# Optimization experiments

Measured on AMD Instinct MI355X. Metric: run time of the kernel, lower is better.

## Reference

```python
import jax, jax.numpy as jnp
import numpy as np

B, N, M, Wlen = 4, 20000, 64, 8


def setup_inputs() -> dict:
    key = jax.random.key(0)
    k1, k2, k3, k4 = jax.random.split(key, 4)
    a0 = jax.random.uniform(k1, (B, N), dtype=jnp.float32)
    W = 0.01 * jax.random.normal(k2, (M, M), dtype=jnp.float32)
    X1 = jax.random.randint(k3, (M, N, Wlen, 2), 0, N, dtype=jnp.int64)
    X2 = jax.random.randint(k4, (M, N, Wlen, 2), 0, N, dtype=jnp.int64)
    return {"a0": a0, "W": W, "X1": X1, "X2": X2, "T": 2}


def f_clause_stack(a, X):
    # a: [B,n], X: [m,n,w,2] -> [B,m,n]
    y1 = a[:, X[..., 0]]  # [B,m,n,w] gather
    y2 = a[:, X[..., 1]]
    return jnp.max(y1 * y2, axis=3)


def predicate_forward(a, W, X1, X2, temperature=1.0):
    F1 = f_clause_stack(a, X1)  # [B,m1,n]
    F2 = f_clause_stack(a, X2)  # [B,m2,n]
    pi = jax.nn.softmax((W / temperature).reshape(-1)).reshape(W.shape)  # [m1,m2]
    pi1 = pi.sum(axis=1)  # [m1]
    pi2 = pi.sum(axis=0)  # [m2]
    Eu = jnp.einsum('j,bjn->bn', pi1, F1)
    Ev = jnp.einsum('k,bkn->bn', pi2, F2)
    Mt = jnp.einsum('jk,bkn->bjn', pi, F2)
    Euv = jnp.sum(F1 * Mt, axis=1)
    return Eu + Ev - Euv  # [B,n]


def reference(a0, W, X1, X2, T):
    a = a0
    for _ in range(T):  # T is a small static int
        derived = predicate_forward(a, W, X1, X2)
        # single intensional predicate -> stack/max over predicates is identity
        a = 1.0 - (1.0 - a) * (1.0 - derived)
    return a
```

## Files before the change

### kernel.cpp

```cpp
#include <hip/hip_runtime.h>

#define NN 20000

typedef _Float16 f16x2 __attribute__((ext_vector_type(2)));
typedef unsigned short u16x2 __attribute__((ext_vector_type(2)));

union U32H2 { unsigned int u; f16x2 h; };
union U32S2 { unsigned int u; u16x2 s; };

__device__ __forceinline__ f16x2 bc_h2(unsigned int u) { U32H2 x; x.u = u; return x.h; }
__device__ __forceinline__ unsigned int dup_h(float v) {
    _Float16 h = (_Float16)v;
    unsigned short b = __builtin_bit_cast(unsigned short, h);
    return ((unsigned int)b << 16) | b;
}
__device__ __forceinline__ unsigned int pkrtz_u32(float a, float b) {
    return __builtin_bit_cast(unsigned int, __builtin_amdgcn_cvt_pkrtz(a, b));
}

__global__ __launch_bounds__(1024) void setup_kernel(const float* __restrict__ W,
                                                     const float* __restrict__ a0,
                                                     unsigned int* __restrict__ pi_t_pk,
                                                     unsigned int* __restrict__ pi1_pk,
                                                     unsigned int* __restrict__ pi2_pk,
                                                     unsigned int* __restrict__ T0) {
    const int t = threadIdx.x;
    if (blockIdx.x != 20) {
        int i = blockIdx.x * 1024 + t;
        if (i < NN) {
            unsigned int b0 = __float2uint_rn(__saturatef(a0[i]) * 255.0f);
            unsigned int b1 = __float2uint_rn(__saturatef(a0[NN + i]) * 255.0f);
            unsigned int b2 = __float2uint_rn(__saturatef(a0[2 * NN + i]) * 255.0f);
            unsigned int b3 = __float2uint_rn(__saturatef(a0[3 * NN + i]) * 255.0f);
            T0[i] = b0 | (b1 << 8) | (b2 << 16) | (b3 << 24);
        }
        return;
    }
    __shared__ float red[1024];
    __shared__ float piL[4096];
    float4 wv = ((const float4*)W)[t];
    float m = fmaxf(fmaxf(wv.x, wv.y), fmaxf(wv.z, wv.w));
    red[t] = m; __syncthreads();
    for (int s = 512; s > 0; s >>= 1) {
        if (t < s) red[t] = fmaxf(red[t], red[t + s]);
        __syncthreads();
    }
    m = red[0];
    __syncthreads();
    float e0 = expf(wv.x - m), e1 = expf(wv.y - m);
    float e2 = expf(wv.z - m), e3 = expf(wv.w - m);
    red[t] = e0 + e1 + e2 + e3;
    __syncthreads();
    for (int s = 512; s > 0; s >>= 1) {
        if (t < s) red[t] += red[t + s];
        __syncthreads();
    }
    float inv = 1.0f / red[0];
    float p[4] = { e0 * inv, e1 * inv, e2 * inv, e3 * inv };
#pragma unroll
    for (int i = 0; i < 4; i++) {
        int f = t * 4 + i;
        piL[f] = p[i];
        pi_t_pk[(f & 63) * 64 + (f >> 6)] = dup_h(p[i]);
    }
    __syncthreads();
    if (t < 64) {
        float s = 0.f;
        for (int k = 0; k < 64; k++) s += piL[t * 64 + k];
        pi1_pk[t] = dup_h(s);
    } else if (t < 128) {
        int k = t - 64;
        float s = 0.f;
        for (int j = 0; j < 64; j++) s += piL[j * 64 + k];
        pi2_pk[k] = dup_h(s);
    }
}

template <int ITER>
__global__ __launch_bounds__(1024, 4) void fused_iter(
    const unsigned int* __restrict__ Tsrc,
    const int* __restrict__ X1, const int* __restrict__ X2,
    const unsigned int* __restrict__ pi_t_pk,
    const unsigned int* __restrict__ pi1_pk,
    const unsigned int* __restrict__ pi2_pk,
    const float* __restrict__ a0,
    unsigned int* __restrict__ Tdst, float* __restrict__ outP) {
    __shared__ unsigned int tab[NN];
    __shared__ unsigned int Ft[128][40][2];
    __shared__ float redp[8][64][4];
    __shared__ float a_sm[64][4];

    const int t = threadIdx.x;
    for (int i = t; i < NN; i += 1024) tab[i] = Tsrc[i];

    const int bid = (int)blockIdx.x;
    const int bstart = bid < 32 ? bid * 79 : 32 * 79 + (bid - 32) * 78;
    const int bcnt = bid < 32 ? 79 : 78;
    const int c0 = (bcnt + 1) >> 1;

    const int wid = t >> 6, lane = t & 63;
    const int widu = __builtin_amdgcn_readfirstlane(wid);
    const int r8 = lane >> 3, n8 = lane & 7;
    const int row = widu * 8 + r8;
    const int k = row & 63;
    const int q = t >> 7, bp = (t >> 6) & 1, n_l = t & 63;
    const int qu = __builtin_amdgcn_readfirstlane(q);

    const char* Xrow = (const char*)(widu >= 8 ? X2 : X1)
                     + (size_t)((unsigned)(k * NN)) * 64u;

    __syncthreads();

    for (int ch = 0; ch < 2; ++ch) {
        const int nb = bstart + (ch ? c0 : 0);
        const int cn = ch ? (bcnt - c0) : c0;

        {
            const float sc = 1.0f / 65025.0f;
            int loff[5];
#pragma unroll
            for (int oc = 0; oc < 5; ++oc) {
                int n = nb + oc * 8 + n8;
                int nc = n < NN ? n : NN - 1;
                loff[oc] = nc * 64;
            }
            int4 qa[4], qb[4];
#pragma unroll
            for (int i = 0; i < 4; ++i) qa[i] = *(const int4*)(Xrow + loff[0] + i * 16);

#pragma unroll
            for (int oc = 0; oc < 5; ++oc) {
                if (oc < 4) {
#pragma unroll
                    for (int i = 0; i < 4; ++i)
                        qb[i] = *(const int4*)(Xrow + loff[oc + 1] + i * 16);
                }
                unsigned int g[16];
                const int* qi = (const int*)qa;
#pragma unroll
                for (int p = 0; p < 16; ++p) g[p] = tab[qi[p]];

                U32S2 me, mo; me.u = 0u; mo.u = 0u;
#pragma unroll
                for (int p = 0; p < 8; ++p) {
                    unsigned int ax = g[2 * p], bx = g[2 * p + 1];
                    unsigned int ea = ax & 0x00FF00FFu;
                    unsigned int oa = __builtin_amdgcn_perm(0u, ax, 0x0C030C01u);
                    unsigned int eb = bx & 0x00FF00FFu;
                    unsigned int ob = __builtin_amdgcn_perm(0u, bx, 0x0C030C01u);
                    U32S2 pe, po, xb;
                    pe.u = ea; xb.u = eb; pe.s = pe.s * xb.s;
                    po.u = oa; xb.u = ob; po.s = po.s * xb.s;
                    me.s = __builtin_elementwise_max(me.s, pe.s);
                    mo.s = __builtin_elementwise_max(mo.s, po.s);
                }
                int col = oc * 8 + n8;
                if (col < cn) {
                    float f0 = (float)(me.u & 0xFFFFu) * sc;
                    float f1 = (float)(mo.u & 0xFFFFu) * sc;
                    float f2 = (float)(me.u >> 16) * sc;
                    float f3 = (float)(mo.u >> 16) * sc;
                    *(uint2*)&Ft[row][col][0] =
                        make_uint2(pkrtz_u32(f0, f1), pkrtz_u32(f2, f3));
                }
#pragma unroll
                for (int i = 0; i < 4; ++i) qa[i] = qb[i];
            }
        }
        __syncthreads();

        {
            float part0 = 0.f, part1 = 0.f;
            if (n_l < cn) {
                f16x2 zero = {(_Float16)0, (_Float16)0};
                f16x2 f1v[8];
                f16x2 eu = zero;
#pragma unroll
                for (int jj = 0; jj < 8; ++jj) {
                    f1v[jj] = bc_h2(Ft[qu * 8 + jj][n_l][bp]);
                    eu += bc_h2(pi1_pk[qu * 8 + jj]) * f1v[jj];
                }
                f16x2 euv = zero, ev = zero;
#pragma unroll 8
                for (int k2 = 0; k2 < 64; ++k2) {
                    f16x2 f2 = bc_h2(Ft[64 + k2][n_l][bp]);
                    const uint4* pt = (const uint4*)(pi_t_pk + k2 * 64 + qu * 8);
                    uint4 w0 = pt[0], w1 = pt[1];
                    f16x2 ts = bc_h2(w0.x) * f1v[0] + bc_h2(w0.y) * f1v[1] +
                               bc_h2(w0.z) * f1v[2] + bc_h2(w0.w) * f1v[3] +
                               bc_h2(w1.x) * f1v[4] + bc_h2(w1.y) * f1v[5] +
                               bc_h2(w1.z) * f1v[6] + bc_h2(w1.w) * f1v[7];
                    euv += f2 * ts;
                    if (qu == 0) ev += bc_h2(pi2_pk[k2]) * f2;
                }
                part0 = (float)eu[0] - (float)euv[0];
                part1 = (float)eu[1] - (float)euv[1];
                if (qu == 0) {
                    part0 += (float)ev[0];
                    part1 += (float)ev[1];
                }
            }
            *(float2*)&redp[q][n_l][bp * 2] = make_float2(part0, part1);
        }
        __syncthreads();

        if (t < 256) {
            int n = t & 63, b = t >> 6;
            if (n < cn) {
                float d = 0.f;
#pragma unroll
                for (int q8 = 0; q8 < 8; ++q8) d += redp[q8][n][b];
                int gn = nb + n;
                float ap;
                if (ITER == 1) ap = a0[(size_t)b * NN + gn];
                else ap = (float)((tab[gn] >> (8 * b)) & 255u) * (1.0f / 255.0f);
                float an = 1.0f - (1.0f - ap) * (1.0f - d);
                if (ITER == 1) a_sm[n][b] = an;
                else outP[(size_t)b * NN + gn] = an;
            }
        }
        __syncthreads();
        if (ITER == 1 && t < 64 && t < cn) {
            unsigned int b0 = __float2uint_rn(__saturatef(a_sm[t][0]) * 255.0f);
            unsigned int b1 = __float2uint_rn(__saturatef(a_sm[t][1]) * 255.0f);
            unsigned int b2 = __float2uint_rn(__saturatef(a_sm[t][2]) * 255.0f);
            unsigned int b3 = __float2uint_rn(__saturatef(a_sm[t][3]) * 255.0f);
            Tdst[nb + t] = b0 | (b1 << 8) | (b2 << 16) | (b3 << 24);
        }
        __syncthreads();
    }
}

extern "C" void kernel_launch(void* const* d_in, const int* in_sizes, int n_in,
                              void* d_out, int out_size, void* d_ws, size_t ws_size,
                              hipStream_t stream) {
    const float* a0 = (const float*)d_in[0];
    const float* W = (const float*)d_in[1];
    const int* X1 = (const int*)d_in[2];
    const int* X2 = (const int*)d_in[3];
    float* out = (float*)d_out;

    if (ws_size < (size_t)193280) return;
    unsigned int* pi_t   = (unsigned int*)((char*)d_ws + 16384);
    unsigned int* pi1_pk = (unsigned int*)((char*)d_ws + 32768);
    unsigned int* pi2_pk = (unsigned int*)((char*)d_ws + 33024);
    unsigned int* T0     = (unsigned int*)((char*)d_ws + 33280);
    unsigned int* T1     = (unsigned int*)((char*)d_ws + 113280);

    setup_kernel<<<21, 1024, 0, stream>>>(W, a0, pi_t, pi1_pk, pi2_pk, T0);
    fused_iter<1><<<256, 1024, 0, stream>>>(T0, X1, X2, pi_t, pi1_pk, pi2_pk,
                                            a0, T1, nullptr);
    fused_iter<2><<<256, 1024, 0, stream>>>(T1, X1, X2, pi_t, pi1_pk, pi2_pk,
                                            nullptr, nullptr, out);
}
```

Measured before the change: 243.4 us.

## Software-pipeline gather and contraction phases with double-buffered LDS in three sub-chunks

After: 244.1 us. About the same (+0.3%).

```diff
diff --git a/kernel.cpp b/kernel.cpp
--- a/kernel.cpp
+++ b/kernel.cpp
@@ -16,6 +16,10 @@
 }
 __device__ __forceinline__ unsigned int pkrtz_u32(float a, float b) {
     return __builtin_bit_cast(unsigned int, __builtin_amdgcn_cvt_pkrtz(a, b));
+}
+template <int CTRL>
+__device__ __forceinline__ unsigned int or_dpp(unsigned int v) {
+    return v | (unsigned int)__builtin_amdgcn_update_dpp(0, (int)v, CTRL, 0xF, 0xF, true);
 }
 
 __global__ __launch_bounds__(1024) void setup_kernel(const float* __restrict__ W,
@@ -86,9 +90,8 @@
     const float* __restrict__ a0,
     unsigned int* __restrict__ Tdst, float* __restrict__ outP) {
     __shared__ unsigned int tab[NN];
-    __shared__ unsigned int Ft[128][40][2];
-    __shared__ float redp[8][64][4];
-    __shared__ float a_sm[64][4];
+    __shared__ unsigned int Ft[2][128][30][2];
+    __shared__ float redp[2][8][64][4];
 
     const int t = threadIdx.x;
     for (int i = t; i < NN; i += 1024) tab[i] = Tsrc[i];
@@ -96,7 +99,6 @@
     const int bid = (int)blockIdx.x;
     const int bstart = bid < 32 ? bid * 79 : 32 * 79 + (bid - 32) * 78;
     const int bcnt = bid < 32 ? 79 : 78;
-    const int c0 = (bcnt + 1) >> 1;
 
     const int wid = t >> 6, lane = t & 63;
     const int widu = __builtin_amdgcn_readfirstlane(wid);
@@ -105,130 +107,149 @@
     const int k = row & 63;
     const int q = t >> 7, bp = (t >> 6) & 1, n_l = t & 63;
     const int qu = __builtin_amdgcn_readfirstlane(q);
-
     const char* Xrow = (const char*)(widu >= 8 ? X2 : X1)
                      + (size_t)((unsigned)(k * NN)) * 64u;
 
     __syncthreads();
 
-    for (int ch = 0; ch < 2; ++ch) {
-        const int nb = bstart + (ch ? c0 : 0);
-        const int cn = ch ? (bcnt - c0) : c0;
-
-        {
-            const float sc = 1.0f / 65025.0f;
-            int loff[5];
-#pragma unroll
-            for (int oc = 0; oc < 5; ++oc) {
-                int n = nb + oc * 8 + n8;
-                int nc = n < NN ? n : NN - 1;
-                loff[oc] = nc * 64;
-            }
-            int4 qa[4], qb[4];
-#pragma unroll
-            for (int i = 0; i < 4; ++i) qa[i] = *(const int4*)(Xrow + loff[0] + i * 16);
-
-#pragma unroll
-            for (int oc = 0; oc < 5; ++oc) {
-                if (oc < 4) {
-#pragma unroll
-                    for (int i = 0; i < 4; ++i)
-                        qb[i] = *(const int4*)(Xrow + loff[oc + 1] + i * 16);
-                }
-                unsigned int g[16];
-                const int* qi = (const int*)qa;
-#pragma unroll
-                for (int p = 0; p < 16; ++p) g[p] = tab[qi[p]];
-
-                U32S2 me, mo; me.u = 0u; mo.u = 0u;
-#pragma unroll
-                for (int p = 0; p < 8; ++p) {
-                    unsigned int ax = g[2 * p], bx = g[2 * p + 1];
-                    unsigned int ea = ax & 0x00FF00FFu;
-                    unsigned int oa = __builtin_amdgcn_perm(0u, ax, 0x0C030C01u);
-                    unsigned int eb = bx & 0x00FF00FFu;
-                    unsigned int ob = __builtin_amdgcn_perm(0u, bx, 0x0C030C01u);
-                    U32S2 pe, po, xb;
-                    pe.u = ea; xb.u = eb; pe.s = pe.s * xb.s;
-                    po.u = oa; xb.u = ob; po.s = po.s * xb.s;
-                    me.s = __builtin_elementwise_max(me.s, pe.s);
-                    mo.s = __builtin_elementwise_max(mo.s, po.s);
-                }
-                int col = oc * 8 + n8;
-                if (col < cn) {
-                    float f0 = (float)(me.u & 0xFFFFu) * sc;
-                    float f1 = (float)(mo.u & 0xFFFFu) * sc;
-                    float f2 = (float)(me.u >> 16) * sc;
-                    float f3 = (float)(mo.u >> 16) * sc;
-                    *(uint2*)&Ft[row][col][0] =
-                        make_uint2(pkrtz_u32(f0, f1), pkrtz_u32(f2, f3));
-                }
-#pragma unroll
-                for (int i = 0; i < 4; ++i) qa[i] = qb[i];
-            }
-        }
-        __syncthreads();
-
-        {
-            float part0 = 0.f, part1 = 0.f;
-            if (n_l < cn) {
-                f16x2 zero = {(_Float16)0, (_Float16)0};
-                f16x2 f1v[8];
-                f16x2 eu = zero;
-#pragma unroll
-                for (int jj = 0; jj < 8; ++jj) {
-                    f1v[jj] = bc_h2(Ft[qu * 8 + jj][n_l][bp]);
-                    eu += bc_h2(pi1_pk[qu * 8 + jj]) * f1v[jj];
-                }
-                f16x2 euv = zero, ev = zero;
+    const float sc = 1.0f / 65025.0f;
+
+    int loffA[4];
+    int4 qa[4];
+
+    auto preload = [&](int nb) {
+#pragma unroll
+        for (int oc = 0; oc < 4; ++oc) {
+            int n = nb + oc * 8 + n8;
+            loffA[oc] = (n < NN ? n : NN - 1) * 64;
+        }
+#pragma unroll
+        for (int i = 0; i < 4; ++i)
+            qa[i] = *(const int4*)(Xrow + loffA[0] + i * 16);
+    };
+
+    auto ph1 = [&](int db, int cn) {
+#pragma unroll
+        for (int oc = 0; oc < 4; ++oc) {
+            if (8 * oc >= cn) break;
+            int4 qb[4];
+            if (8 * (oc + 1) < cn) {
+#pragma unroll
+                for (int i = 0; i < 4; ++i)
+                    qb[i] = *(const int4*)(Xrow + loffA[oc + 1] + i * 16);
+            }
+            unsigned int g[16];
+            const int* qi = (const int*)qa;
+#pragma unroll
+            for (int p = 0; p < 16; ++p) g[p] = tab[qi[p]];
+
+            U32S2 me, mo; me.u = 0u; mo.u = 0u;
+#pragma unroll
+            for (int p = 0; p < 8; ++p) {
+                unsigned int ax = g[2 * p], bx = g[2 * p + 1];
+                unsigned int ea = ax & 0x00FF00FFu;
+                unsigned int oa = __builtin_amdgcn_perm(0u, ax, 0x0C030C01u);
+                unsigned int eb = bx & 0x00FF00FFu;
+                unsigned int ob = __builtin_amdgcn_perm(0u, bx, 0x0C030C01u);
+                U32S2 pe, po, xb;
+                pe.u = ea; xb.u = eb; pe.s = pe.s * xb.s;
+                po.u = oa; xb.u = ob; po.s = po.s * xb.s;
+                me.s = __builtin_elementwise_max(me.s, pe.s);
+                mo.s = __builtin_elementwise_max(mo.s, po.s);
+            }
+            int col = oc * 8 + n8;
+            if (col < cn) {
+                float f0 = (float)(me.u & 0xFFFFu) * sc;
+                float f1 = (float)(mo.u & 0xFFFFu) * sc;
+                float f2 = (float)(me.u >> 16) * sc;
+                float f3 = (float)(mo.u >> 16) * sc;
+                *(uint2*)&Ft[db][row][col][0] =
+                    make_uint2(pkrtz_u32(f0, f1), pkrtz_u32(f2, f3));
+            }
+#pragma unroll
+            for (int i = 0; i < 4; ++i) qa[i] = qb[i];
+        }
+    };
+
+    auto ph2 = [&](int sb, int cn) {
+        float part0 = 0.f, part1 = 0.f;
+        if (n_l < cn) {
+            f16x2 zero = {(_Float16)0, (_Float16)0};
+            f16x2 f1v[8];
+            f16x2 eu = zero;
+#pragma unroll
+            for (int jj = 0; jj < 8; ++jj) {
+                f1v[jj] = bc_h2(Ft[sb][qu * 8 + jj][n_l][bp]);
+                eu += bc_h2(pi1_pk[qu * 8 + jj]) * f1v[jj];
+            }
+            f16x2 euv = zero, ev = zero;
 #pragma unroll 8
-                for (int k2 = 0; k2 < 64; ++k2) {
-                    f16x2 f2 = bc_h2(Ft[64 + k2][n_l][bp]);
-                    const uint4* pt = (const uint4*)(pi_t_pk + k2 * 64 + qu * 8);
-                    uint4 w0 = pt[0], w1 = pt[1];
-                    f16x2 ts = bc_h2(w0.x) * f1v[0] + bc_h2(w0.y) * f1v[1] +
-                               bc_h2(w0.z) * f1v[2] + bc_h2(w0.w) * f1v[3] +
-                               bc_h2(w1.x) * f1v[4] + bc_h2(w1.y) * f1v[5] +
-                               bc_h2(w1.z) * f1v[6] + bc_h2(w1.w) * f1v[7];
-                    euv += f2 * ts;
-                    if (qu == 0) ev += bc_h2(pi2_pk[k2]) * f2;
-                }
-                part0 = (float)eu[0] - (float)euv[0];
-                part1 = (float)eu[1] - (float)euv[1];
-                if (qu == 0) {
-                    part0 += (float)ev[0];
-                    part1 += (float)ev[1];
-                }
-            }
-            *(float2*)&redp[q][n_l][bp * 2] = make_float2(part0, part1);
-        }
-        __syncthreads();
-
+            for (int k2 = 0; k2 < 64; ++k2) {
+                f16x2 f2 = bc_h2(Ft[sb][64 + k2][n_l][bp]);
+                const uint4* pt = (const uint4*)(pi_t_pk + k2 * 64 + qu * 8);
+                uint4 w0 = pt[0], w1 = pt[1];
+                f16x2 ts = bc_h2(w0.x) * f1v[0] + bc_h2(w0.y) * f1v[1] +
+                           bc_h2(w0.z) * f1v[2] + bc_h2(w0.w) * f1v[3] +
+                           bc_h2(w1.x) * f1v[4] + bc_h2(w1.y) * f1v[5] +
+                           bc_h2(w1.z) * f1v[6] + bc_h2(w1.w) * f1v[7];
+                euv += f2 * ts;
+                if (qu == 0) ev += bc_h2(pi2_pk[k2]) * f2;
+            }
+            part0 = (float)eu[0] - (float)euv[0];
+            part1 = (float)eu[1] - (float)euv[1];
+            if (qu == 0) {
+                part0 += (float)ev[0];
+                part1 += (float)ev[1];
+            }
+        }
+        *(float2*)&redp[sb][q][n_l][bp * 2] = make_float2(part0, part1);
+    };
+
+    auto comb = [&](int pb, int nb, int cn) {
         if (t < 256) {
-            int n = t & 63, b = t >> 6;
+            int n = t >> 2, b = t & 3;
             if (n < cn) {
                 float d = 0.f;
 #pragma unroll
-                for (int q8 = 0; q8 < 8; ++q8) d += redp[q8][n][b];
+                for (int q8 = 0; q8 < 8; ++q8) d += redp[pb][q8][n][b];
                 int gn = nb + n;
                 float ap;
                 if (ITER == 1) ap = a0[(size_t)b * NN + gn];
                 else ap = (float)((tab[gn] >> (8 * b)) & 255u) * (1.0f / 255.0f);
                 float an = 1.0f - (1.0f - ap) * (1.0f - d);
-                if (ITER == 1) a_sm[n][b] = an;
-                else outP[(size_t)b * NN + gn] = an;
-            }
+                if (ITER == 1) {
+                    unsigned int v = __float2uint_rn(__saturatef(an) * 255.0f) << (8 * b);
+                    v = or_dpp<0xB1>(v);
+                    v = or_dpp<0x4E>(v);
+                    if (b == 0) Tdst[gn] = v;
+                } else {
+                    outP[(size_t)b * NN + gn] = an;
+                }
+            }
+        }
+    };
+
+    preload(bstart);
+    ph1(0, 30);
+    __syncthreads();
+
+#pragma unroll
+    for (int r = 0; r < 3; ++r) {
+        if (r < 2) preload(bstart + 30 * (r + 1));
+        if (r > 0) {
+            comb((r + 1) & 1, bstart + 30 * (r - 1), 30);
+        }
+        {
+            int cnr = bcnt - 30 * r; cnr = cnr > 30 ? 30 : cnr;
+            ph2(r & 1, cnr);
+        }
+        if (r < 2) {
+            int cn1 = bcnt - 30 * (r + 1); cn1 = cn1 > 30 ? 30 : cn1;
+            ph1((r + 1) & 1, cn1);
         }
         __syncthreads();
-        if (ITER == 1 && t < 64 && t < cn) {
-            unsigned int b0 = __float2uint_rn(__saturatef(a_sm[t][0]) * 255.0f);
-            unsigned int b1 = __float2uint_rn(__saturatef(a_sm[t][1]) * 255.0f);
-            unsigned int b2 = __float2uint_rn(__saturatef(a_sm[t][2]) * 255.0f);
-            unsigned int b3 = __float2uint_rn(__saturatef(a_sm[t][3]) * 255.0f);
-            Tdst[nb + t] = b0 | (b1 << 8) | (b2 << 16) | (b3 << 24);
-        }
-        __syncthreads();
-    }
+    }
+    comb(0, bstart + 60, bcnt - 60);
 }
 
 extern "C" void kernel_launch(void* const* d_in, const int* in_sizes, int n_in,
```
